# Optimization experiments

Measured on AMD Instinct MI355X. Metric: run time of the kernel, lower is better.

Reference implementation:

```python
import jax, jax.numpy as jnp
import numpy as np

MAX_COV = 1e4
MIN_COV = 1e-4
SYMM_THRESH = 1e-5
DET_THRESH = 1e-6
MAX_POS = 1e3
EIG_CLAMP = 1e-4
INV_EPS = 1e-4


def _symmetrize(A):
    return (A + jnp.swapaxes(A, -1, -2)) * 0.5


def _spd_reconstruct(Q, lam):
    # Q @ diag(lam) @ Q^T for batched [N,3,3] Q and [N,3] lam
    return jnp.einsum('bij,bj,bkj->bik', Q, lam, Q)


def setup_inputs() -> dict:
    key = jax.random.key(0)
    k1, k2, k3, k4 = jax.random.split(key, 4)
    N = 1048576
    miu_1 = jax.random.normal(k1, (N, 3), dtype=jnp.float32)
    miu_2 = jax.random.normal(k2, (N, 3), dtype=jnp.float32)
    I = jnp.eye(3, dtype=jnp.float32)
    B1 = 0.5 * jax.random.normal(k3, (N, 3, 3), dtype=jnp.float32)
    B2 = 0.5 * jax.random.normal(k4, (N, 3, 3), dtype=jnp.float32)
    cov_1 = jnp.einsum('bij,bkj->bik', B1, B1) + 0.3 * I
    cov_2 = jnp.einsum('bij,bkj->bik', B2, B2) + 0.3 * I
    return {'miu_1': miu_1, 'miu_2': miu_2, 'cov_1': cov_1, 'cov_2': cov_2}


def _stable_mask(miu_1, miu_2, cov_1, cov_2):
    a1 = jnp.abs(cov_1)
    a2 = jnp.abs(cov_2)
    m = (a1.max((-1, -2)) < MAX_COV) & (a2.max((-1, -2)) < MAX_COV)
    m &= (a1.min((-1, -2)) > MIN_COV) & (a2.min((-1, -2)) > MIN_COV)
    d1 = jnp.abs(cov_1 - jnp.swapaxes(cov_1, -1, -2)).max((-1, -2))
    d2 = jnp.abs(cov_2 - jnp.swapaxes(cov_2, -1, -2)).max((-1, -2))
    m &= (d1 < SYMM_THRESH) & (d2 < SYMM_THRESH)
    m &= (jnp.abs(jnp.linalg.det(cov_1)) > DET_THRESH)
    m &= (jnp.abs(jnp.linalg.det(cov_2)) > DET_THRESH)
    m &= jnp.all(jnp.isfinite(cov_1), axis=(-1, -2))
    m &= jnp.all(jnp.isfinite(cov_2), axis=(-1, -2))
    m &= jnp.abs(miu_1).max(-1) < MAX_POS
    m &= jnp.abs(miu_2).max(-1) < MAX_POS
    return m


def reference(miu_1, miu_2, cov_1, cov_2):
    mask = _stable_mask(miu_1, miu_2, cov_1, cov_2)  # [N] bool
    mM = mask[:, None, None]
    I = jnp.eye(3, dtype=cov_1.dtype)
    # sanitize masked-out rows so eigh stays well-conditioned; their outputs
    # are overwritten with zeros below (matching torch's masked-index path)
    c1 = jnp.where(mM, cov_1, I)
    c2 = jnp.where(mM, cov_2, I)

    L_A, Q_A = jnp.linalg.eigh(_symmetrize(c1))
    L_A = jnp.maximum(L_A, EIG_CLAMP)
    sqrt_L = jnp.sqrt(L_A)
    A_sqrt = _spd_reconstruct(Q_A, sqrt_L)               # cov1^{1/2}
    A_sqrt_inv = _spd_reconstruct(Q_A, 1.0 / (INV_EPS + sqrt_L))

    C = _symmetrize(jnp.einsum('bij,bjk,blk->bil', A_sqrt, c2, A_sqrt))
    L_C, Q_C = jnp.linalg.eigh(C)
    C_sqrt = _spd_reconstruct(Q_C, (L_C ** 2) ** 0.25)   # matrix_sqrt_H

    cov_vel = jnp.einsum('bij,bjk,blk->bil', A_sqrt, C_sqrt, A_sqrt_inv)
    cov_vel = cov_vel + jnp.swapaxes(cov_vel, -1, -2) - cov_1 - jnp.swapaxes(cov_1, -1, -2)

    miu_vel = jnp.where(mask[:, None], miu_2 - miu_1, 0.0)
    cov_vel = jnp.where(mM, cov_vel, 0.0)
    return miu_vel, cov_vel
```

## Files before the change

kernel.cpp:

```cpp
#include <hip/hip_runtime.h>
#include <math.h>

#define MAX_COV 10000.0f
#define MIN_COV 0.0001f
#define SYMM_THRESH 1e-05f
#define DET_THRESH 1e-06f
#define MAX_POS 1000.0f
#define EIG_CLAMP 0.0001f
#define INV_EPS 0.0001f

namespace {
constexpr int BS = 256;

__device__ __forceinline__ float rcp_fast(float x)  { return __builtin_amdgcn_rcpf(x); }
__device__ __forceinline__ float sqrt_fast(float x) { return __builtin_amdgcn_sqrtf(x); }

__device__ __forceinline__ float acos_fast(float x) {
    const float t = fabsf(x);
    const float s = sqrt_fast(fmaxf(1.0f - t, 0.0f));
    float p = fmaf(t, -0.0187293f, 0.0742610f);
    p = fmaf(t, p, -0.2121144f);
    p = fmaf(t, p, 1.5707288f);
    const float a = s * p;
    return (x >= 0.0f) ? a : (3.14159265358979f - a);
}

__device__ __forceinline__ void eigvals3(
    float m00, float m01, float m02, float m11, float m12, float m22,
    float& l1, float& l2, float& l3)
{
    const float q   = (m00 + m11 + m22) * (1.0f / 3.0f);
    const float b00 = m00 - q, b11 = m11 - q, b22 = m22 - q;
    const float offsq = m01 * m01 + m02 * m02 + m12 * m12;
    const float p2  = b00 * b00 + b11 * b11 + b22 * b22 + 2.0f * offsq;
    const float p   = sqrt_fast(p2 * (1.0f / 6.0f));
    const float detB =
          b00 * (b11 * b22 - m12 * m12)
        - m01 * (m01 * b22 - m12 * m02)
        + m02 * (m01 * m12 - b11 * m02);
    const float pinv = rcp_fast(fmaxf(p, 1e-30f));
    float r = 0.5f * detB;
    r = r * pinv; r = r * pinv; r = r * pinv;
    r = fminf(1.0f, fmaxf(-1.0f, r));
    const float phi = acos_fast(r) * (1.0f / 3.0f);
    const float c   = __cosf(phi);
    const float s   = sqrt_fast(fmaxf(1.0f - c * c, 0.0f));
    l1 = q + 2.0f * p * c;
    l3 = q + p * (-c - 1.7320508075688772f * s);
    l2 = 3.0f * q - l1 - l3;
}

__global__ __launch_bounds__(BS, 4)
void wl_kernel(const float* __restrict__ miu1, const float* __restrict__ miu2,
               const float* __restrict__ cov1, const float* __restrict__ cov2,
               float* __restrict__ out, int N)
{
    const int i = blockIdx.x * BS + threadIdx.x;
    if (i >= N) return;

    float c1[9], c2r[9], u1[3], u2[3];
    {
        const float* p1 = cov1 + (size_t)i * 9;
        const float* p2 = cov2 + (size_t)i * 9;
        #pragma unroll
        for (int k = 0; k < 9; ++k) { c1[k] = p1[k]; c2r[k] = p2[k]; }
        const float* q1p = miu1 + (size_t)i * 3;
        const float* q2p = miu2 + (size_t)i * 3;
        #pragma unroll
        for (int k = 0; k < 3; ++k) { u1[k] = q1p[k]; u2[k] = q2p[k]; }
    }

    float amax1 = 0.0f, amax2 = 0.0f, amin1 = 1e30f, amin2 = 1e30f;
    #pragma unroll
    for (int k = 0; k < 9; ++k) {
        amax1 = fmaxf(amax1, fabsf(c1[k]));  amin1 = fminf(amin1, fabsf(c1[k]));
        amax2 = fmaxf(amax2, fabsf(c2r[k])); amin2 = fminf(amin2, fabsf(c2r[k]));
    }
    bool ok = (amax1 < MAX_COV) && (amax2 < MAX_COV)
           && (amin1 > MIN_COV) && (amin2 > MIN_COV);
    const float sd = fmaxf(fmaxf(fabsf(c1[1] - c1[3]), fabsf(c1[2] - c1[6])),
                    fmaxf(fabsf(c1[5] - c1[7]),
                    fmaxf(fmaxf(fabsf(c2r[1] - c2r[3]), fabsf(c2r[2] - c2r[6])),
                          fabsf(c2r[5] - c2r[7]))));
    ok = ok && (sd < SYMM_THRESH);
    const float det1 = c1[0] * (c1[4] * c1[8] - c1[5] * c1[7])
                     - c1[1] * (c1[3] * c1[8] - c1[5] * c1[6])
                     + c1[2] * (c1[3] * c1[7] - c1[4] * c1[6]);
    const float det2 = c2r[0] * (c2r[4] * c2r[8] - c2r[5] * c2r[7])
                     - c2r[1] * (c2r[3] * c2r[8] - c2r[5] * c2r[6])
                     + c2r[2] * (c2r[3] * c2r[7] - c2r[4] * c2r[6]);
    ok = ok && (fabsf(det1) > DET_THRESH) && (fabsf(det2) > DET_THRESH);
    const float um = fmaxf(fmaxf(fmaxf(fabsf(u1[0]), fabsf(u1[1])), fabsf(u1[2])),
                           fmaxf(fmaxf(fabsf(u2[0]), fabsf(u2[1])), fabsf(u2[2])));
    ok = ok && (um < MAX_POS);

    const float m00 = ok ? c1[0] : 1.0f;
    const float m01 = ok ? (0.5f * (c1[1] + c1[3])) : 0.0f;
    const float m02 = ok ? (0.5f * (c1[2] + c1[6])) : 0.0f;
    const float m11 = ok ? c1[4] : 1.0f;
    const float m12 = ok ? (0.5f * (c1[5] + c1[7])) : 0.0f;
    const float m22 = ok ? c1[8] : 1.0f;
    const float d00 = ok ? c2r[0] : 1.0f;
    const float d01 = ok ? (0.5f * (c2r[1] + c2r[3])) : 0.0f;
    const float d02 = ok ? (0.5f * (c2r[2] + c2r[6])) : 0.0f;
    const float d11 = ok ? c2r[4] : 1.0f;
    const float d12 = ok ? (0.5f * (c2r[5] + c2r[7])) : 0.0f;
    const float d22 = ok ? c2r[8] : 1.0f;

    float l1, l2, l3;
    eigvals3(m00, m01, m02, m11, m12, m22, l1, l2, l3);
    l1 = fmaxf(l1, EIG_CLAMP); l2 = fmaxf(l2, EIG_CLAMP); l3 = fmaxf(l3, EIG_CLAMP);
    const float sa = sqrt_fast(l1), sb = sqrt_fast(l2), sc = sqrt_fast(l3);
    const float i_ab = rcp_fast(sa + sb);
    const float i_bc = rcp_fast(sb + sc);
    const float i_ac = rcp_fast(sa + sc);
    const float q0 = sa, q1 = i_ab, q2 = -i_ab * i_bc * i_ac;
    const float ea = rcp_fast(INV_EPS + sa);
    const float eb = rcp_fast(INV_EPS + sb);
    const float ec = rcp_fast(INV_EPS + sc);
    const float g0 = ea;
    const float g1 = -ea * eb * i_ab;
    const float g2 = (INV_EPS + sa + sb + sc) * ea * eb * ec * i_ab * i_bc * i_ac;

    const float u00 = m00 - l1, u11 = m11 - l1, u22 = m22 - l1;
    const float v00 = m00 - l2, v11 = m11 - l2, v22 = m22 - l2;
    const float P00 = u00 * v00 + m01 * m01 + m02 * m02;
    const float P01 = u00 * m01 + m01 * v11 + m02 * m12;
    const float P02 = u00 * m02 + m01 * m12 + m02 * v22;
    const float P11 = m01 * m01 + u11 * v11 + m12 * m12;
    const float P12 = m01 * m02 + u11 * m12 + m12 * v22;
    const float P22 = m02 * m02 + m12 * m12 + u22 * v22;

    const float S00 = q0 + q1 * u00 + q2 * P00;
    const float S01 =      q1 * m01 + q2 * P01;
    const float S02 =      q1 * m02 + q2 * P02;
    const float S11 = q0 + q1 * u11 + q2 * P11;
    const float S12 =      q1 * m12 + q2 * P12;
    const float S22 = q0 + q1 * u22 + q2 * P22;

    const float G00 = g0 + g1 * u00 + g2 * P00;
    const float G01 =      g1 * m01 + g2 * P01;
    const float G02 =      g1 * m02 + g2 * P02;
    const float G11 = g0 + g1 * u11 + g2 * P11;
    const float G12 =      g1 * m12 + g2 * P12;
    const float G22 = g0 + g1 * u22 + g2 * P22;

    const float T00 = S00 * d00 + S01 * d01 + S02 * d02;
    const float T01 = S00 * d01 + S01 * d11 + S02 * d12;
    const float T02 = S00 * d02 + S01 * d12 + S02 * d22;
    const float T10 = S01 * d00 + S11 * d01 + S12 * d02;
    const float T11 = S01 * d01 + S11 * d11 + S12 * d12;
    const float T12 = S01 * d02 + S11 * d12 + S12 * d22;
    const float T20 = S02 * d00 + S12 * d01 + S22 * d02;
    const float T21 = S02 * d01 + S12 * d11 + S22 * d12;
    const float T22m = S02 * d02 + S12 * d12 + S22 * d22;
    const float C00 = T00 * S00 + T01 * S01 + T02 * S02;
    const float C01 = T00 * S01 + T01 * S11 + T02 * S12;
    const float C02 = T00 * S02 + T01 * S12 + T02 * S22;
    const float C11 = T10 * S01 + T11 * S11 + T12 * S12;
    const float C12 = T10 * S02 + T11 * S12 + T12 * S22;
    const float C22 = T20 * S02 + T21 * S12 + T22m * S22;

    float e1, e2, e3;
    eigvals3(C00, C01, C02, C11, C12, C22, e1, e2, e3);
    const float ra = sqrt_fast(fabsf(e1));
    const float rb = sqrt_fast(fabsf(e2));
    const float rc = sqrt_fast(fabsf(e3));
    const float j_ab = rcp_fast(fmaxf(ra + rb, 1e-12f));
    const float j_bc = rcp_fast(fmaxf(rb + rc, 1e-12f));
    const float j_ac = rcp_fast(fmaxf(ra + rc, 1e-12f));
    const float h0 = ra, h1 = j_ab, h2 = -j_ab * j_bc * j_ac;
    const float cu00 = C00 - e1, cu11 = C11 - e1, cu22 = C22 - e1;
    const float cv00 = C00 - e2, cv11 = C11 - e2, cv22 = C22 - e2;
    const float R00 = cu00 * cv00 + C01 * C01 + C02 * C02;
    const float R01 = cu00 * C01 + C01 * cv11 + C02 * C12;
    const float R02 = cu00 * C02 + C01 * C12 + C02 * cv22;
    const float R11 = C01 * C01 + cu11 * cv11 + C12 * C12;
    const float R12 = C01 * C02 + cu11 * C12 + C12 * cv22;
    const float R22 = C02 * C02 + C12 * C12 + cu22 * cv22;

    const float X00 = h0 + h1 * cu00 + h2 * R00;
    const float X01 =      h1 * C01  + h2 * R01;
    const float X02 =      h1 * C02  + h2 * R02;
    const float X11 = h0 + h1 * cu11 + h2 * R11;
    const float X12 =      h1 * C12  + h2 * R12;
    const float X22 = h0 + h1 * cu22 + h2 * R22;

    const float A00 = S00 * X00 + S01 * X01 + S02 * X02;
    const float A01 = S00 * X01 + S01 * X11 + S02 * X12;
    const float A02 = S00 * X02 + S01 * X12 + S02 * X22;
    const float A10 = S01 * X00 + S11 * X01 + S12 * X02;
    const float A11 = S01 * X01 + S11 * X11 + S12 * X12;
    const float A12 = S01 * X02 + S11 * X12 + S12 * X22;
    const float A20 = S02 * X00 + S12 * X01 + S22 * X02;
    const float A21 = S02 * X01 + S12 * X11 + S22 * X12;
    const float A22 = S02 * X02 + S12 * X12 + S22 * X22;
    float W[9];
    W[0] = A00 * G00 + A01 * G01 + A02 * G02;
    W[1] = A00 * G01 + A01 * G11 + A02 * G12;
    W[2] = A00 * G02 + A01 * G12 + A02 * G22;
    W[3] = A10 * G00 + A11 * G01 + A12 * G02;
    W[4] = A10 * G01 + A11 * G11 + A12 * G12;
    W[5] = A10 * G02 + A11 * G12 + A12 * G22;
    W[6] = A20 * G00 + A21 * G01 + A22 * G02;
    W[7] = A20 * G01 + A21 * G11 + A22 * G12;
    W[8] = A20 * G02 + A21 * G12 + A22 * G22;

    const float M1f[9] = { m00, m01, m02, m01, m11, m12, m02, m12, m22 };
    float* out_miu = out;
    float* out_cov = out + (size_t)N * 3;
    float* oc = out_cov + (size_t)i * 9;
    #pragma unroll
    for (int r = 0; r < 3; ++r)
        #pragma unroll
        for (int cidx = 0; cidx < 3; ++cidx)
            oc[r * 3 + cidx] = ok ? (W[r * 3 + cidx] + W[cidx * 3 + r] - 2.0f * M1f[r * 3 + cidx])
                                  : 0.0f;
    float* om = out_miu + (size_t)i * 3;
    #pragma unroll
    for (int k = 0; k < 3; ++k) om[k] = ok ? (u2[k] - u1[k]) : 0.0f;
}

}

extern "C" void kernel_launch(void* const* d_in, const int* in_sizes, int n_in,
                              void* d_out, int out_size, void* d_ws, size_t ws_size,
                              hipStream_t stream)
{
    const float* miu1 = (const float*)d_in[0];
    const float* miu2 = (const float*)d_in[1];
    const float* cov1 = (const float*)d_in[2];
    const float* cov2 = (const float*)d_in[3];
    float* out = (float*)d_out;
    const int N = in_sizes[0] / 3;
    const int grid = (N + BS - 1) / BS;
    hipLaunchKernelGGL(wl_kernel, dim3(grid), dim3(BS), 0, stream,
                       miu1, miu2, cov1, cov2, out, N);
}
```

Before: 28.61 us.

## Stage covariance loads and stores through LDS with coalesced float4 transfers

Each block now loads its 256x9 covariance tiles for both inputs into shared memory with coalesced float4 global reads, computes per-thread from LDS, writes the results back into LDS, and then stores them with coalesced float4 writes. This replaces the strided 36-byte-per-thread global accesses that produced poorly coalesced memory transactions. The occupancy hint is also raised from 4 to 8 blocks. The cost is 18 KB of LDS per block, two barriers, possible LDS bank conflicts from the stride-9 per-thread access, and register pressure from the tighter launch bound.

```diff
diff --git a/kernel.cpp b/kernel.cpp
--- a/kernel.cpp
+++ b/kernel.cpp
@@ -50,175 +50,214 @@
     l2 = 3.0f * q - l1 - l3;
 }
 
-__global__ __launch_bounds__(BS, 4)
+__global__ __launch_bounds__(BS, 8)
 void wl_kernel(const float* __restrict__ miu1, const float* __restrict__ miu2,
                const float* __restrict__ cov1, const float* __restrict__ cov2,
                float* __restrict__ out, int N)
 {
-    const int i = blockIdx.x * BS + threadIdx.x;
-    if (i >= N) return;
-
-    float c1[9], c2r[9], u1[3], u2[3];
-    {
-        const float* p1 = cov1 + (size_t)i * 9;
-        const float* p2 = cov2 + (size_t)i * 9;
-        #pragma unroll
-        for (int k = 0; k < 9; ++k) { c1[k] = p1[k]; c2r[k] = p2[k]; }
-        const float* q1p = miu1 + (size_t)i * 3;
-        const float* q2p = miu2 + (size_t)i * 3;
-        #pragma unroll
-        for (int k = 0; k < 3; ++k) { u1[k] = q1p[k]; u2[k] = q2p[k]; }
+    __shared__ float s_a[BS * 9];
+    __shared__ float s_b[BS * 9];
+
+    const int tid  = threadIdx.x;
+    const int base = blockIdx.x * BS;
+    const int nb   = min(BS, N - base);
+    const bool full = (nb == BS);
+
+    float* out_cov = out + (size_t)N * 3;
+
+    if (full) {
+        const float4* g1 = (const float4*)(cov1 + (size_t)base * 9);
+        const float4* g2 = (const float4*)(cov2 + (size_t)base * 9);
+        float4* la = (float4*)s_a;
+        float4* lb = (float4*)s_b;
+        #pragma unroll
+        for (int j = 0; j < 2; ++j) {
+            la[tid + j * BS] = g1[tid + j * BS];
+            lb[tid + j * BS] = g2[tid + j * BS];
+        }
+        if (tid < BS * 9 / 4 - 2 * BS) {
+            la[2 * BS + tid] = g1[2 * BS + tid];
+            lb[2 * BS + tid] = g2[2 * BS + tid];
+        }
+    } else {
+        for (int j = tid; j < nb * 9; j += BS) {
+            s_a[j] = cov1[(size_t)base * 9 + j];
+            s_b[j] = cov2[(size_t)base * 9 + j];
+        }
     }
-
-    float amax1 = 0.0f, amax2 = 0.0f, amin1 = 1e30f, amin2 = 1e30f;
-    #pragma unroll
-    for (int k = 0; k < 9; ++k) {
-        amax1 = fmaxf(amax1, fabsf(c1[k]));  amin1 = fminf(amin1, fabsf(c1[k]));
-        amax2 = fmaxf(amax2, fabsf(c2r[k])); amin2 = fminf(amin2, fabsf(c2r[k]));
+    __syncthreads();
+
+    if (tid < nb) {
+        const int i = base + tid;
+        float c1[9], c2r[9], u1[3], u2[3];
+        #pragma unroll
+        for (int k = 0; k < 9; ++k) { c1[k] = s_a[tid * 9 + k]; c2r[k] = s_b[tid * 9 + k]; }
+        {
+            const float* q1p = miu1 + (size_t)i * 3;
+            const float* q2p = miu2 + (size_t)i * 3;
+            #pragma unroll
+            for (int k = 0; k < 3; ++k) { u1[k] = q1p[k]; u2[k] = q2p[k]; }
+        }
+
+        float amax1 = 0.0f, amax2 = 0.0f, amin1 = 1e30f, amin2 = 1e30f;
+        #pragma unroll
+        for (int k = 0; k < 9; ++k) {
+            amax1 = fmaxf(amax1, fabsf(c1[k]));  amin1 = fminf(amin1, fabsf(c1[k]));
+            amax2 = fmaxf(amax2, fabsf(c2r[k])); amin2 = fminf(amin2, fabsf(c2r[k]));
+        }
+        bool ok = (amax1 < MAX_COV) && (amax2 < MAX_COV)
+               && (amin1 > MIN_COV) && (amin2 > MIN_COV);
+        const float sd = fmaxf(fmaxf(fabsf(c1[1] - c1[3]), fabsf(c1[2] - c1[6])),
+                        fmaxf(fabsf(c1[5] - c1[7]),
+                        fmaxf(fmaxf(fabsf(c2r[1] - c2r[3]), fabsf(c2r[2] - c2r[6])),
+                              fabsf(c2r[5] - c2r[7]))));
+        ok = ok && (sd < SYMM_THRESH);
+        const float det1 = c1[0] * (c1[4] * c1[8] - c1[5] * c1[7])
+                         - c1[1] * (c1[3] * c1[8] - c1[5] * c1[6])
+                         + c1[2] * (c1[3] * c1[7] - c1[4] * c1[6]);
+        const float det2 = c2r[0] * (c2r[4] * c2r[8] - c2r[5] * c2r[7])
+                         - c2r[1] * (c2r[3] * c2r[8] - c2r[5] * c2r[6])
+                         + c2r[2] * (c2r[3] * c2r[7] - c2r[4] * c2r[6]);
+        ok = ok && (fabsf(det1) > DET_THRESH) && (fabsf(det2) > DET_THRESH);
+        const float um = fmaxf(fmaxf(fmaxf(fabsf(u1[0]), fabsf(u1[1])), fabsf(u1[2])),
+                               fmaxf(fmaxf(fabsf(u2[0]), fabsf(u2[1])), fabsf(u2[2])));
+        ok = ok && (um < MAX_POS);
+
+        const float m00 = ok ? c1[0] : 1.0f;
+        const float m01 = ok ? (0.5f * (c1[1] + c1[3])) : 0.0f;
+        const float m02 = ok ? (0.5f * (c1[2] + c1[6])) : 0.0f;
+        const float m11 = ok ? c1[4] : 1.0f;
+        const float m12 = ok ? (0.5f * (c1[5] + c1[7])) : 0.0f;
+        const float m22 = ok ? c1[8] : 1.0f;
+        const float d00 = ok ? c2r[0] : 1.0f;
+        const float d01 = ok ? (0.5f * (c2r[1] + c2r[3])) : 0.0f;
+        const float d02 = ok ? (0.5f * (c2r[2] + c2r[6])) : 0.0f;
+        const float d11 = ok ? c2r[4] : 1.0f;
+        const float d12 = ok ? (0.5f * (c2r[5] + c2r[7])) : 0.0f;
+        const float d22 = ok ? c2r[8] : 1.0f;
+
+        float l1, l2, l3;
+        eigvals3(m00, m01, m02, m11, m12, m22, l1, l2, l3);
+        l1 = fmaxf(l1, EIG_CLAMP); l2 = fmaxf(l2, EIG_CLAMP); l3 = fmaxf(l3, EIG_CLAMP);
+        const float sa = sqrt_fast(l1), sb = sqrt_fast(l2), sc = sqrt_fast(l3);
+        const float i_ab = rcp_fast(sa + sb);
+        const float i_bc = rcp_fast(sb + sc);
+        const float i_ac = rcp_fast(sa + sc);
+        const float q0 = sa, q1 = i_ab, q2 = -i_ab * i_bc * i_ac;
+        const float ea = rcp_fast(INV_EPS + sa);
+        const float eb = rcp_fast(INV_EPS + sb);
+        const float ec = rcp_fast(INV_EPS + sc);
+        const float g0 = ea;
+        const float g1 = -ea * eb * i_ab;
+        const float g2 = (INV_EPS + sa + sb + sc) * ea * eb * ec * i_ab * i_bc * i_ac;
+
+        const float u00 = m00 - l1, u11 = m11 - l1, u22 = m22 - l1;
+        const float v00 = m00 - l2, v11 = m11 - l2, v22 = m22 - l2;
+        const float P00 = u00 * v00 + m01 * m01 + m02 * m02;
+        const float P01 = u00 * m01 + m01 * v11 + m02 * m12;
+        const float P02 = u00 * m02 + m01 * m12 + m02 * v22;
+        const float P11 = m01 * m01 + u11 * v11 + m12 * m12;
+        const float P12 = m01 * m02 + u11 * m12 + m12 * v22;
+        const float P22 = m02 * m02 + m12 * m12 + u22 * v22;
+
+        const float S00 = q0 + q1 * u00 + q2 * P00;
+        const float S01 =      q1 * m01 + q2 * P01;
+        const float S02 =      q1 * m02 + q2 * P02;
+        const float S11 = q0 + q1 * u11 + q2 * P11;
+        const float S12 =      q1 * m12 + q2 * P12;
+        const float S22 = q0 + q1 * u22 + q2 * P22;
+
+        const float G00 = g0 + g1 * u00 + g2 * P00;
+        const float G01 =      g1 * m01 + g2 * P01;
+        const float G02 =      g1 * m02 + g2 * P02;
+        const float G11 = g0 + g1 * u11 + g2 * P11;
+        const float G12 =      g1 * m12 + g2 * P12;
+        const float G22 = g0 + g1 * u22 + g2 * P22;
+
+        const float T00 = S00 * d00 + S01 * d01 + S02 * d02;
+        const float T01 = S00 * d01 + S01 * d11 + S02 * d12;
+        const float T02 = S00 * d02 + S01 * d12 + S02 * d22;
+        const float T10 = S01 * d00 + S11 * d01 + S12 * d02;
+        const float T11 = S01 * d01 + S11 * d11 + S12 * d12;
+        const float T12 = S01 * d02 + S11 * d12 + S12 * d22;
+        const float T20 = S02 * d00 + S12 * d01 + S22 * d02;
+        const float T21 = S02 * d01 + S12 * d11 + S22 * d12;
+        const float T22m = S02 * d02 + S12 * d12 + S22 * d22;
+        const float C00 = T00 * S00 + T01 * S01 + T02 * S02;
+        const float C01 = T00 * S01 + T01 * S11 + T02 * S12;
+        const float C02 = T00 * S02 + T01 * S12 + T02 * S22;
+        const float C11 = T10 * S01 + T11 * S11 + T12 * S12;
+        const float C12 = T10 * S02 + T11 * S12 + T12 * S22;
+        const float C22 = T20 * S02 + T21 * S12 + T22m * S22;
+
+        float e1, e2, e3;
+        eigvals3(C00, C01, C02, C11, C12, C22, e1, e2, e3);
+        const float ra = sqrt_fast(fabsf(e1));
+        const float rb = sqrt_fast(fabsf(e2));
+        const float rc = sqrt_fast(fabsf(e3));
+        const float j_ab = rcp_fast(fmaxf(ra + rb, 1e-12f));
+        const float j_bc = rcp_fast(fmaxf(rb + rc, 1e-12f));
+        const float j_ac = rcp_fast(fmaxf(ra + rc, 1e-12f));
+        const float h0 = ra, h1 = j_ab, h2 = -j_ab * j_bc * j_ac;
+        const float cu00 = C00 - e1, cu11 = C11 - e1, cu22 = C22 - e1;
+        const float cv00 = C00 - e2, cv11 = C11 - e2, cv22 = C22 - e2;
+        const float R00 = cu00 * cv00 + C01 * C01 + C02 * C02;
+        const float R01 = cu00 * C01 + C01 * cv11 + C02 * C12;
+        const float R02 = cu00 * C02 + C01 * C12 + C02 * cv22;
+        const float R11 = C01 * C01 + cu11 * cv11 + C12 * C12;
+        const float R12 = C01 * C02 + cu11 * C12 + C12 * cv22;
+        const float R22 = C02 * C02 + C12 * C12 + cu22 * cv22;
+
+        const float X00 = h0 + h1 * cu00 + h2 * R00;
+        const float X01 =      h1 * C01  + h2 * R01;
+        const float X02 =      h1 * C02  + h2 * R02;
+        const float X11 = h0 + h1 * cu11 + h2 * R11;
+        const float X12 =      h1 * C12  + h2 * R12;
+        const float X22 = h0 + h1 * cu22 + h2 * R22;
+
+        const float A00 = S00 * X00 + S01 * X01 + S02 * X02;
+        const float A01 = S00 * X01 + S01 * X11 + S02 * X12;
+        const float A02 = S00 * X02 + S01 * X12 + S02 * X22;
+        const float A10 = S01 * X00 + S11 * X01 + S12 * X02;
+        const float A11 = S01 * X01 + S11 * X11 + S12 * X12;
+        const float A12 = S01 * X02 + S11 * X12 + S12 * X22;
+        const float A20 = S02 * X00 + S12 * X01 + S22 * X02;
+        const float A21 = S02 * X01 + S12 * X11 + S22 * X12;
+        const float A22 = S02 * X02 + S12 * X12 + S22 * X22;
+        float W[9];
+        W[0] = A00 * G00 + A01 * G01 + A02 * G02;
+        W[1] = A00 * G01 + A01 * G11 + A02 * G12;
+        W[2] = A00 * G02 + A01 * G12 + A02 * G22;
+        W[3] = A10 * G00 + A11 * G01 + A12 * G02;
+        W[4] = A10 * G01 + A11 * G11 + A12 * G12;
+        W[5] = A10 * G02 + A11 * G12 + A12 * G22;
+        W[6] = A20 * G00 + A21 * G01 + A22 * G02;
+        W[7] = A20 * G01 + A21 * G11 + A22 * G12;
+        W[8] = A20 * G02 + A21 * G12 + A22 * G22;
+
+        const float M1f[9] = { m00, m01, m02, m01, m11, m12, m02, m12, m22 };
+        #pragma unroll
+        for (int r = 0; r < 3; ++r)
+            #pragma unroll
+            for (int cidx = 0; cidx < 3; ++cidx)
+                s_a[tid * 9 + r * 3 + cidx] =
+                    ok ? (W[r * 3 + cidx] + W[cidx * 3 + r] - 2.0f * M1f[r * 3 + cidx]) : 0.0f;
+
+        float* om = out + (size_t)i * 3;
+        #pragma unroll
+        for (int k = 0; k < 3; ++k) om[k] = ok ? (u2[k] - u1[k]) : 0.0f;
     }
-    bool ok = (amax1 < MAX_COV) && (amax2 < MAX_COV)
-           && (amin1 > MIN_COV) && (amin2 > MIN_COV);
-    const float sd = fmaxf(fmaxf(fabsf(c1[1] - c1[3]), fabsf(c1[2] - c1[6])),
-                    fmaxf(fabsf(c1[5] - c1[7]),
-                    fmaxf(fmaxf(fabsf(c2r[1] - c2r[3]), fabsf(c2r[2] - c2r[6])),
-                          fabsf(c2r[5] - c2r[7]))));
-    ok = ok && (sd < SYMM_THRESH);
-    const float det1 = c1[0] * (c1[4] * c1[8] - c1[5] * c1[7])
-                     - c1[1] * (c1[3] * c1[8] - c1[5] * c1[6])
-                     + c1[2] * (c1[3] * c1[7] - c1[4] * c1[6]);
-    const float det2 = c2r[0] * (c2r[4] * c2r[8] - c2r[5] * c2r[7])
-                     - c2r[1] * (c2r[3] * c2r[8] - c2r[5] * c2r[6])
-                     + c2r[2] * (c2r[3] * c2r[7] - c2r[4] * c2r[6]);
-    ok = ok && (fabsf(det1) > DET_THRESH) && (fabsf(det2) > DET_THRESH);
-    const float um = fmaxf(fmaxf(fmaxf(fabsf(u1[0]), fabsf(u1[1])), fabsf(u1[2])),
-                           fmaxf(fmaxf(fabsf(u2[0]), fabsf(u2[1])), fabsf(u2[2])));
-    ok = ok && (um < MAX_POS);
-
-    const float m00 = ok ? c1[0] : 1.0f;
-    const float m01 = ok ? (0.5f * (c1[1] + c1[3])) : 0.0f;
-    const float m02 = ok ? (0.5f * (c1[2] + c1[6])) : 0.0f;
-    const float m11 = ok ? c1[4] : 1.0f;
-    const float m12 = ok ? (0.5f * (c1[5] + c1[7])) : 0.0f;
-    const float m22 = ok ? c1[8] : 1.0f;
-    const float d00 = ok ? c2r[0] : 1.0f;
-    const float d01 = ok ? (0.5f * (c2r[1] + c2r[3])) : 0.0f;
-    const float d02 = ok ? (0.5f * (c2r[2] + c2r[6])) : 0.0f;
-    const float d11 = ok ? c2r[4] : 1.0f;
-    const float d12 = ok ? (0.5f * (c2r[5] + c2r[7])) : 0.0f;
-    const float d22 = ok ? c2r[8] : 1.0f;
-
-    float l1, l2, l3;
-    eigvals3(m00, m01, m02, m11, m12, m22, l1, l2, l3);
-    l1 = fmaxf(l1, EIG_CLAMP); l2 = fmaxf(l2, EIG_CLAMP); l3 = fmaxf(l3, EIG_CLAMP);
-    const float sa = sqrt_fast(l1), sb = sqrt_fast(l2), sc = sqrt_fast(l3);
-    const float i_ab = rcp_fast(sa + sb);
-    const float i_bc = rcp_fast(sb + sc);
-    const float i_ac = rcp_fast(sa + sc);
-    const float q0 = sa, q1 = i_ab, q2 = -i_ab * i_bc * i_ac;
-    const float ea = rcp_fast(INV_EPS + sa);
-    const float eb = rcp_fast(INV_EPS + sb);
-    const float ec = rcp_fast(INV_EPS + sc);
-    const float g0 = ea;
-    const float g1 = -ea * eb * i_ab;
-    const float g2 = (INV_EPS + sa + sb + sc) * ea * eb * ec * i_ab * i_bc * i_ac;
-
-    const float u00 = m00 - l1, u11 = m11 - l1, u22 = m22 - l1;
-    const float v00 = m00 - l2, v11 = m11 - l2, v22 = m22 - l2;
-    const float P00 = u00 * v00 + m01 * m01 + m02 * m02;
-    const float P01 = u00 * m01 + m01 * v11 + m02 * m12;
-    const float P02 = u00 * m02 + m01 * m12 + m02 * v22;
-    const float P11 = m01 * m01 + u11 * v11 + m12 * m12;
-    const float P12 = m01 * m02 + u11 * m12 + m12 * v22;
-    const float P22 = m02 * m02 + m12 * m12 + u22 * v22;
-
-    const float S00 = q0 + q1 * u00 + q2 * P00;
-    const float S01 =      q1 * m01 + q2 * P01;
-    const float S02 =      q1 * m02 + q2 * P02;
-    const float S11 = q0 + q1 * u11 + q2 * P11;
-    const float S12 =      q1 * m12 + q2 * P12;
-    const float S22 = q0 + q1 * u22 + q2 * P22;
-
-    const float G00 = g0 + g1 * u00 + g2 * P00;
-    const float G01 =      g1 * m01 + g2 * P01;
-    const float G02 =      g1 * m02 + g2 * P02;
-    const float G11 = g0 + g1 * u11 + g2 * P11;
-    const float G12 =      g1 * m12 + g2 * P12;
-    const float G22 = g0 + g1 * u22 + g2 * P22;
-
-    const float T00 = S00 * d00 + S01 * d01 + S02 * d02;
-    const float T01 = S00 * d01 + S01 * d11 + S02 * d12;
-    const float T02 = S00 * d02 + S01 * d12 + S02 * d22;
-    const float T10 = S01 * d00 + S11 * d01 + S12 * d02;
-    const float T11 = S01 * d01 + S11 * d11 + S12 * d12;
-    const float T12 = S01 * d02 + S11 * d12 + S12 * d22;
-    const float T20 = S02 * d00 + S12 * d01 + S22 * d02;
-    const float T21 = S02 * d01 + S12 * d11 + S22 * d12;
-    const float T22m = S02 * d02 + S12 * d12 + S22 * d22;
-    const float C00 = T00 * S00 + T01 * S01 + T02 * S02;
-    const float C01 = T00 * S01 + T01 * S11 + T02 * S12;
-    const float C02 = T00 * S02 + T01 * S12 + T02 * S22;
-    const float C11 = T10 * S01 + T11 * S11 + T12 * S12;
-    const float C12 = T10 * S02 + T11 * S12 + T12 * S22;
-    const float C22 = T20 * S02 + T21 * S12 + T22m * S22;
-
-    float e1, e2, e3;
-    eigvals3(C00, C01, C02, C11, C12, C22, e1, e2, e3);
-    const float ra = sqrt_fast(fabsf(e1));
-    const float rb = sqrt_fast(fabsf(e2));
-    const float rc = sqrt_fast(fabsf(e3));
-    const float j_ab = rcp_fast(fmaxf(ra + rb, 1e-12f));
-    const float j_bc = rcp_fast(fmaxf(rb + rc, 1e-12f));
-    const float j_ac = rcp_fast(fmaxf(ra + rc, 1e-12f));
-    const float h0 = ra, h1 = j_ab, h2 = -j_ab * j_bc * j_ac;
-    const float cu00 = C00 - e1, cu11 = C11 - e1, cu22 = C22 - e1;
-    const float cv00 = C00 - e2, cv11 = C11 - e2, cv22 = C22 - e2;
-    const float R00 = cu00 * cv00 + C01 * C01 + C02 * C02;
-    const float R01 = cu00 * C01 + C01 * cv11 + C02 * C12;
-    const float R02 = cu00 * C02 + C01 * C12 + C02 * cv22;
-    const float R11 = C01 * C01 + cu11 * cv11 + C12 * C12;
-    const float R12 = C01 * C02 + cu11 * C12 + C12 * cv22;
-    const float R22 = C02 * C02 + C12 * C12 + cu22 * cv22;
-
-    const float X00 = h0 + h1 * cu00 + h2 * R00;
-    const float X01 =      h1 * C01  + h2 * R01;
-    const float X02 =      h1 * C02  + h2 * R02;
-    const float X11 = h0 + h1 * cu11 + h2 * R11;
-    const float X12 =      h1 * C12  + h2 * R12;
-    const float X22 = h0 + h1 * cu22 + h2 * R22;
-
-    const float A00 = S00 * X00 + S01 * X01 + S02 * X02;
-    const float A01 = S00 * X01 + S01 * X11 + S02 * X12;
-    const float A02 = S00 * X02 + S01 * X12 + S02 * X22;
-    const float A10 = S01 * X00 + S11 * X01 + S12 * X02;
-    const float A11 = S01 * X01 + S11 * X11 + S12 * X12;
-    const float A12 = S01 * X02 + S11 * X12 + S12 * X22;
-    const float A20 = S02 * X00 + S12 * X01 + S22 * X02;
-    const float A21 = S02 * X01 + S12 * X11 + S22 * X12;
-    const float A22 = S02 * X02 + S12 * X12 + S22 * X22;
-    float W[9];
-    W[0] = A00 * G00 + A01 * G01 + A02 * G02;
-    W[1] = A00 * G01 + A01 * G11 + A02 * G12;
-    W[2] = A00 * G02 + A01 * G12 + A02 * G22;
-    W[3] = A10 * G00 + A11 * G01 + A12 * G02;
-    W[4] = A10 * G01 + A11 * G11 + A12 * G12;
-    W[5] = A10 * G02 + A11 * G12 + A12 * G22;
-    W[6] = A20 * G00 + A21 * G01 + A22 * G02;
-    W[7] = A20 * G01 + A21 * G11 + A22 * G12;
-    W[8] = A20 * G02 + A21 * G12 + A22 * G22;
-
-    const float M1f[9] = { m00, m01, m02, m01, m11, m12, m02, m12, m22 };
-    float* out_miu = out;
-    float* out_cov = out + (size_t)N * 3;
-    float* oc = out_cov + (size_t)i * 9;
-    #pragma unroll
-    for (int r = 0; r < 3; ++r)
-        #pragma unroll
-        for (int cidx = 0; cidx < 3; ++cidx)
-            oc[r * 3 + cidx] = ok ? (W[r * 3 + cidx] + W[cidx * 3 + r] - 2.0f * M1f[r * 3 + cidx])
-                                  : 0.0f;
-    float* om = out_miu + (size_t)i * 3;
-    #pragma unroll
-    for (int k = 0; k < 3; ++k) om[k] = ok ? (u2[k] - u1[k]) : 0.0f;
+    __syncthreads();
+
+    if (full && ((((size_t)(out_cov + (size_t)base * 9)) & 15) == 0)) {
+        float4* go = (float4*)(out_cov + (size_t)base * 9);
+        const float4* la = (const float4*)s_a;
+        #pragma unroll
+        for (int j = 0; j < 2; ++j) go[tid + j * BS] = la[tid + j * BS];
+        if (tid < BS * 9 / 4 - 2 * BS) go[2 * BS + tid] = la[2 * BS + tid];
+    } else {
+        for (int j = tid; j < nb * 9; j += BS) out_cov[(size_t)base * 9 + j] = s_a[j];
+    }
 }
 
 }
```

Result: slower. 39.52 us (+38.1%).

## Stage per-wave loads and stores through LDS for coalesced global access

Applied to the files above, without the earlier changes.

Each wave now copies its 64 elements' covariance and mean data into shared memory with coalesced contiguous loads, then each lane reads its own strided record from LDS. Outputs go back through LDS the same way before coalesced global stores. This targets the uncoalesced 9-float and 3-float strided accesses of the per-thread layout, at the cost of about 18 KB of LDS per block, extra LDS traffic and possible bank conflicts on the stride-9 and stride-3 reads. A tail path keeps the direct per-thread access for partial waves.

```diff
diff --git a/kernel.cpp b/kernel.cpp
--- a/kernel.cpp
+++ b/kernel.cpp
@@ -11,6 +11,7 @@
 
 namespace {
 constexpr int BS = 256;
+constexpr int NW = BS / 64;
 
 __device__ __forceinline__ float rcp_fast(float x)  { return __builtin_amdgcn_rcpf(x); }
 __device__ __forceinline__ float sqrt_fast(float x) { return __builtin_amdgcn_sqrtf(x); }
@@ -50,26 +51,10 @@
     l2 = 3.0f * q - l1 - l3;
 }
 
-__global__ __launch_bounds__(BS, 4)
-void wl_kernel(const float* __restrict__ miu1, const float* __restrict__ miu2,
-               const float* __restrict__ cov1, const float* __restrict__ cov2,
-               float* __restrict__ out, int N)
-{
-    const int i = blockIdx.x * BS + threadIdx.x;
-    if (i >= N) return;
-
-    float c1[9], c2r[9], u1[3], u2[3];
-    {
-        const float* p1 = cov1 + (size_t)i * 9;
-        const float* p2 = cov2 + (size_t)i * 9;
-        #pragma unroll
-        for (int k = 0; k < 9; ++k) { c1[k] = p1[k]; c2r[k] = p2[k]; }
-        const float* q1p = miu1 + (size_t)i * 3;
-        const float* q2p = miu2 + (size_t)i * 3;
-        #pragma unroll
-        for (int k = 0; k < 3; ++k) { u1[k] = q1p[k]; u2[k] = q2p[k]; }
-    }
-
+__device__ __forceinline__ void process_one(
+    const float* c1, const float* c2r, const float* u1, const float* u2,
+    float* wout, float* mv)
+{
     float amax1 = 0.0f, amax2 = 0.0f, amin1 = 1e30f, amin2 = 1e30f;
     #pragma unroll
     for (int k = 0; k < 9; ++k) {
@@ -207,18 +192,90 @@
     W[8] = A20 * G02 + A21 * G12 + A22 * G22;
 
     const float M1f[9] = { m00, m01, m02, m01, m11, m12, m02, m12, m22 };
-    float* out_miu = out;
-    float* out_cov = out + (size_t)N * 3;
-    float* oc = out_cov + (size_t)i * 9;
     #pragma unroll
     for (int r = 0; r < 3; ++r)
         #pragma unroll
         for (int cidx = 0; cidx < 3; ++cidx)
-            oc[r * 3 + cidx] = ok ? (W[r * 3 + cidx] + W[cidx * 3 + r] - 2.0f * M1f[r * 3 + cidx])
-                                  : 0.0f;
-    float* om = out_miu + (size_t)i * 3;
+            wout[r * 3 + cidx] =
+                ok ? (W[r * 3 + cidx] + W[cidx * 3 + r] - 2.0f * M1f[r * 3 + cidx]) : 0.0f;
     #pragma unroll
-    for (int k = 0; k < 3; ++k) om[k] = ok ? (u2[k] - u1[k]) : 0.0f;
+    for (int k = 0; k < 3; ++k) mv[k] = ok ? (u2[k] - u1[k]) : 0.0f;
+}
+
+__global__ __launch_bounds__(BS, 4)
+void wl_kernel(const float* __restrict__ miu1, const float* __restrict__ miu2,
+               const float* __restrict__ cov1, const float* __restrict__ cov2,
+               float* __restrict__ out, int N)
+{
+    __shared__ float s_c1[NW][576];
+    __shared__ float s_c2[NW][576];
+    __shared__ float s_mu[NW][384];
+
+    const int w = threadIdx.x >> 6;
+    const int l = threadIdx.x & 63;
+    const int wbase = blockIdx.x * BS + w * 64;
+    if (wbase >= N) return;
+
+    float* out_cov = out + (size_t)N * 3;
+    float c1[9], c2[9], u1[3], u2[3];
+    float wout[9], mv[3];
+
+    if (wbase + 64 <= N) {
+        const float* g1 = cov1 + (size_t)wbase * 9;
+        const float* g2 = cov2 + (size_t)wbase * 9;
+        #pragma unroll
+        for (int k = 0; k < 9; ++k) {
+            s_c1[w][l + 64 * k] = g1[l + 64 * k];
+            s_c2[w][l + 64 * k] = g2[l + 64 * k];
+        }
+        const float* gm1 = miu1 + (size_t)wbase * 3;
+        const float* gm2 = miu2 + (size_t)wbase * 3;
+        #pragma unroll
+        for (int k = 0; k < 3; ++k) {
+            s_mu[w][l + 64 * k]       = gm1[l + 64 * k];
+            s_mu[w][192 + l + 64 * k] = gm2[l + 64 * k];
+        }
+        __builtin_amdgcn_wave_barrier();
+
+        #pragma unroll
+        for (int k = 0; k < 9; ++k) { c1[k] = s_c1[w][l * 9 + k]; c2[k] = s_c2[w][l * 9 + k]; }
+        #pragma unroll
+        for (int k = 0; k < 3; ++k) { u1[k] = s_mu[w][l * 3 + k]; u2[k] = s_mu[w][192 + l * 3 + k]; }
+
+        process_one(c1, c2, u1, u2, wout, mv);
+
+        __builtin_amdgcn_wave_barrier();
+        #pragma unroll
+        for (int k = 0; k < 9; ++k) s_c1[w][l * 9 + k] = wout[k];
+        #pragma unroll
+        for (int k = 0; k < 3; ++k) s_mu[w][l * 3 + k] = mv[k];
+        __builtin_amdgcn_wave_barrier();
+
+        float* oc = out_cov + (size_t)wbase * 9;
+        #pragma unroll
+        for (int k = 0; k < 9; ++k) oc[l + 64 * k] = s_c1[w][l + 64 * k];
+        float* om = out + (size_t)wbase * 3;
+        #pragma unroll
+        for (int k = 0; k < 3; ++k) om[l + 64 * k] = s_mu[w][l + 64 * k];
+    } else {
+        const int i = wbase + l;
+        if (i >= N) return;
+        #pragma unroll
+        for (int k = 0; k < 9; ++k) {
+            c1[k] = cov1[(size_t)i * 9 + k];
+            c2[k] = cov2[(size_t)i * 9 + k];
+        }
+        #pragma unroll
+        for (int k = 0; k < 3; ++k) {
+            u1[k] = miu1[(size_t)i * 3 + k];
+            u2[k] = miu2[(size_t)i * 3 + k];
+        }
+        process_one(c1, c2, u1, u2, wout, mv);
+        #pragma unroll
+        for (int k = 0; k < 9; ++k) out_cov[(size_t)i * 9 + k] = wout[k];
+        #pragma unroll
+        for (int k = 0; k < 3; ++k) out[(size_t)i * 3 + k] = mv[k];
+    }
 }
 
 }
```

New measurement: 29.52 us. 1.03x slower.

## Pack per-thread 3x3 matrix math into float2 vectors for packed FMA

Applied to the files above, without the earlier changes.

Rewrites the per-element matrix products (P, S/G, T, C, R, X, A, W and the output symmetrisation) as operations on two-wide float vectors, so the compiler can emit packed FP32 instructions (v_pk_fma_f32) that do two lanes per instruction. It also folds the divide-by-three into the acos polynomial coefficients, computes pinv cubed once, and replaces the sqrt(1-c^2) with __sinf. The aim is to cut VALU instruction count in a compute-bound kernel. The cost is extra register shuffles to build and split the vectors, which may offset the gain, plus small accuracy changes from the refit polynomial and __sinf.

```diff
diff --git a/kernel.cpp b/kernel.cpp
--- a/kernel.cpp
+++ b/kernel.cpp
@@ -12,17 +12,20 @@
 namespace {
 constexpr int BS = 256;
 
+typedef float v2f __attribute__((ext_vector_type(2)));
+__device__ __forceinline__ v2f mk2(float a, float b) { v2f r; r[0] = a; r[1] = b; return r; }
+
 __device__ __forceinline__ float rcp_fast(float x)  { return __builtin_amdgcn_rcpf(x); }
 __device__ __forceinline__ float sqrt_fast(float x) { return __builtin_amdgcn_sqrtf(x); }
 
-__device__ __forceinline__ float acos_fast(float x) {
+__device__ __forceinline__ float acos3_fast(float x) {
     const float t = fabsf(x);
     const float s = sqrt_fast(fmaxf(1.0f - t, 0.0f));
-    float p = fmaf(t, -0.0187293f, 0.0742610f);
-    p = fmaf(t, p, -0.2121144f);
-    p = fmaf(t, p, 1.5707288f);
-    const float a = s * p;
-    return (x >= 0.0f) ? a : (3.14159265358979f - a);
+    float p = fmaf(t, -0.00624310f, 0.02475367f);
+    p = fmaf(t, p, -0.07070480f);
+    p = fmaf(t, p, 0.52357627f);
+    const float a3 = s * p;
+    return (x >= 0.0f) ? a3 : (1.0471975512f - a3);
 }
 
 __device__ __forceinline__ void eigvals3(
@@ -38,13 +41,13 @@
           b00 * (b11 * b22 - m12 * m12)
         - m01 * (m01 * b22 - m12 * m02)
         + m02 * (m01 * m12 - b11 * m02);
-    const float pinv = rcp_fast(fmaxf(p, 1e-30f));
-    float r = 0.5f * detB;
-    r = r * pinv; r = r * pinv; r = r * pinv;
+    const float pinv  = rcp_fast(fmaxf(p, 1e-30f));
+    const float pinv3 = pinv * pinv * pinv;
+    float r = (0.5f * detB) * pinv3;
     r = fminf(1.0f, fmaxf(-1.0f, r));
-    const float phi = acos_fast(r) * (1.0f / 3.0f);
+    const float phi = acos3_fast(r);
     const float c   = __cosf(phi);
-    const float s   = sqrt_fast(fmaxf(1.0f - c * c, 0.0f));
+    const float s   = __sinf(phi);
     l1 = q + 2.0f * p * c;
     l3 = q + p * (-c - 1.7320508075688772f * s);
     l2 = 3.0f * q - l1 - l3;
@@ -94,18 +97,21 @@
                            fmaxf(fmaxf(fabsf(u2[0]), fabsf(u2[1])), fabsf(u2[2])));
     ok = ok && (um < MAX_POS);
 
+    const v2f md01 = 0.5f * (mk2(c1[1], c2r[1]) + mk2(c1[3], c2r[3]));
+    const v2f md02 = 0.5f * (mk2(c1[2], c2r[2]) + mk2(c1[6], c2r[6]));
+    const v2f md12 = 0.5f * (mk2(c1[5], c2r[5]) + mk2(c1[7], c2r[7]));
     const float m00 = ok ? c1[0] : 1.0f;
-    const float m01 = ok ? (0.5f * (c1[1] + c1[3])) : 0.0f;
-    const float m02 = ok ? (0.5f * (c1[2] + c1[6])) : 0.0f;
     const float m11 = ok ? c1[4] : 1.0f;
-    const float m12 = ok ? (0.5f * (c1[5] + c1[7])) : 0.0f;
     const float m22 = ok ? c1[8] : 1.0f;
+    const float m01 = ok ? md01[0] : 0.0f;
+    const float m02 = ok ? md02[0] : 0.0f;
+    const float m12 = ok ? md12[0] : 0.0f;
     const float d00 = ok ? c2r[0] : 1.0f;
-    const float d01 = ok ? (0.5f * (c2r[1] + c2r[3])) : 0.0f;
-    const float d02 = ok ? (0.5f * (c2r[2] + c2r[6])) : 0.0f;
     const float d11 = ok ? c2r[4] : 1.0f;
-    const float d12 = ok ? (0.5f * (c2r[5] + c2r[7])) : 0.0f;
     const float d22 = ok ? c2r[8] : 1.0f;
+    const float d01 = ok ? md01[1] : 0.0f;
+    const float d02 = ok ? md02[1] : 0.0f;
+    const float d12 = ok ? md12[1] : 0.0f;
 
     float l1, l2, l3;
     eigvals3(m00, m01, m02, m11, m12, m22, l1, l2, l3);
@@ -114,52 +120,50 @@
     const float i_ab = rcp_fast(sa + sb);
     const float i_bc = rcp_fast(sb + sc);
     const float i_ac = rcp_fast(sa + sc);
-    const float q0 = sa, q1 = i_ab, q2 = -i_ab * i_bc * i_ac;
     const float ea = rcp_fast(INV_EPS + sa);
     const float eb = rcp_fast(INV_EPS + sb);
     const float ec = rcp_fast(INV_EPS + sc);
-    const float g0 = ea;
-    const float g1 = -ea * eb * i_ab;
-    const float g2 = (INV_EPS + sa + sb + sc) * ea * eb * ec * i_ab * i_bc * i_ac;
+    const v2f qg0 = mk2(sa, ea);
+    const v2f qg1 = mk2(i_ab, -ea * eb * i_ab);
+    const v2f qg2 = mk2(-i_ab * i_bc * i_ac,
+                        (INV_EPS + sa + sb + sc) * ea * eb * ec * i_ab * i_bc * i_ac);
 
     const float u00 = m00 - l1, u11 = m11 - l1, u22 = m22 - l1;
     const float v00 = m00 - l2, v11 = m11 - l2, v22 = m22 - l2;
-    const float P00 = u00 * v00 + m01 * m01 + m02 * m02;
-    const float P01 = u00 * m01 + m01 * v11 + m02 * m12;
-    const float P02 = u00 * m02 + m01 * m12 + m02 * v22;
-    const float P11 = m01 * m01 + u11 * v11 + m12 * m12;
-    const float P12 = m01 * m02 + u11 * m12 + m12 * v22;
-    const float P22 = m02 * m02 + m12 * m12 + u22 * v22;
-
-    const float S00 = q0 + q1 * u00 + q2 * P00;
-    const float S01 =      q1 * m01 + q2 * P01;
-    const float S02 =      q1 * m02 + q2 * P02;
-    const float S11 = q0 + q1 * u11 + q2 * P11;
-    const float S12 =      q1 * m12 + q2 * P12;
-    const float S22 = q0 + q1 * u22 + q2 * P22;
-
-    const float G00 = g0 + g1 * u00 + g2 * P00;
-    const float G01 =      g1 * m01 + g2 * P01;
-    const float G02 =      g1 * m02 + g2 * P02;
-    const float G11 = g0 + g1 * u11 + g2 * P11;
-    const float G12 =      g1 * m12 + g2 * P12;
-    const float G22 = g0 + g1 * u22 + g2 * P22;
-
-    const float T00 = S00 * d00 + S01 * d01 + S02 * d02;
-    const float T01 = S00 * d01 + S01 * d11 + S02 * d12;
-    const float T02 = S00 * d02 + S01 * d12 + S02 * d22;
-    const float T10 = S01 * d00 + S11 * d01 + S12 * d02;
-    const float T11 = S01 * d01 + S11 * d11 + S12 * d12;
-    const float T12 = S01 * d02 + S11 * d12 + S12 * d22;
-    const float T20 = S02 * d00 + S12 * d01 + S22 * d02;
-    const float T21 = S02 * d01 + S12 * d11 + S22 * d12;
-    const float T22m = S02 * d02 + S12 * d12 + S22 * d22;
-    const float C00 = T00 * S00 + T01 * S01 + T02 * S02;
-    const float C01 = T00 * S01 + T01 * S11 + T02 * S12;
-    const float C02 = T00 * S02 + T01 * S12 + T02 * S22;
-    const float C11 = T10 * S01 + T11 * S11 + T12 * S12;
-    const float C12 = T10 * S02 + T11 * S12 + T12 * S22;
-    const float C22 = T20 * S02 + T21 * S12 + T22m * S22;
+    const v2f PA = u00 * mk2(v00, m01) + m01 * mk2(m01, v11) + m02 * mk2(m02, m12);
+    const v2f PB = mk2(u00, m01) * mk2(m02, m01) + mk2(m01, u11) * mk2(m12, v11)
+                 + mk2(m02, m12) * mk2(v22, m12);
+    const v2f PC = mk2(m01, m02) * mk2(m02, m02) + mk2(u11, m12) * mk2(m12, m12)
+                 + mk2(m12, u22) * mk2(v22, v22);
+
+    const v2f SG00 = qg0 + qg1 * u00 + qg2 * PA[0];
+    const v2f SG01 =       qg1 * m01 + qg2 * PA[1];
+    const v2f SG02 =       qg1 * m02 + qg2 * PB[0];
+    const v2f SG11 = qg0 + qg1 * u11 + qg2 * PB[1];
+    const v2f SG12 =       qg1 * m12 + qg2 * PC[0];
+    const v2f SG22 = qg0 + qg1 * u22 + qg2 * PC[1];
+    const float S00 = SG00[0], G00 = SG00[1];
+    const float S01 = SG01[0], G01 = SG01[1];
+    const float S02 = SG02[0], G02 = SG02[1];
+    const float S11 = SG11[0], G11 = SG11[1];
+    const float S12 = SG12[0], G12 = SG12[1];
+    const float S22 = SG22[0], G22 = SG22[1];
+
+    const v2f TA = S00 * mk2(d00, d01) + S01 * mk2(d01, d11) + S02 * mk2(d02, d12);
+    const v2f TB = mk2(S00, S01) * mk2(d02, d00) + mk2(S01, S11) * mk2(d12, d01)
+                 + mk2(S02, S12) * mk2(d22, d02);
+    const v2f TC = S01 * mk2(d01, d02) + S11 * mk2(d11, d12) + S12 * mk2(d12, d22);
+    const v2f TD = S02 * mk2(d00, d01) + S12 * mk2(d01, d11) + S22 * mk2(d02, d12);
+    const float T00 = TA[0], T01 = TA[1], T02 = TB[0], T10 = TB[1];
+    const float T11 = TC[0], T12 = TC[1], T20 = TD[0], T21 = TD[1];
+    const float T22 = S02 * d02 + S12 * d12 + S22 * d22;
+
+    const v2f CA = T00 * mk2(S00, S01) + T01 * mk2(S01, S11) + T02 * mk2(S02, S12);
+    const v2f CB = mk2(T00, T10) * mk2(S02, S01) + mk2(T01, T11) * mk2(S12, S11)
+                 + mk2(T02, T12) * mk2(S22, S12);
+    const v2f CC = mk2(T10, T20) * S02 + mk2(T11, T21) * S12 + mk2(T12, T22) * S22;
+    const float C00 = CA[0], C01 = CA[1], C02 = CB[0];
+    const float C11 = CB[1], C12 = CC[0], C22 = CC[1];
 
     float e1, e2, e3;
     eigvals3(C00, C01, C02, C11, C12, C22, e1, e2, e3);
@@ -172,51 +176,52 @@
     const float h0 = ra, h1 = j_ab, h2 = -j_ab * j_bc * j_ac;
     const float cu00 = C00 - e1, cu11 = C11 - e1, cu22 = C22 - e1;
     const float cv00 = C00 - e2, cv11 = C11 - e2, cv22 = C22 - e2;
-    const float R00 = cu00 * cv00 + C01 * C01 + C02 * C02;
-    const float R01 = cu00 * C01 + C01 * cv11 + C02 * C12;
-    const float R02 = cu00 * C02 + C01 * C12 + C02 * cv22;
-    const float R11 = C01 * C01 + cu11 * cv11 + C12 * C12;
-    const float R12 = C01 * C02 + cu11 * C12 + C12 * cv22;
-    const float R22 = C02 * C02 + C12 * C12 + cu22 * cv22;
-
-    const float X00 = h0 + h1 * cu00 + h2 * R00;
-    const float X01 =      h1 * C01  + h2 * R01;
-    const float X02 =      h1 * C02  + h2 * R02;
-    const float X11 = h0 + h1 * cu11 + h2 * R11;
-    const float X12 =      h1 * C12  + h2 * R12;
-    const float X22 = h0 + h1 * cu22 + h2 * R22;
-
-    const float A00 = S00 * X00 + S01 * X01 + S02 * X02;
-    const float A01 = S00 * X01 + S01 * X11 + S02 * X12;
-    const float A02 = S00 * X02 + S01 * X12 + S02 * X22;
-    const float A10 = S01 * X00 + S11 * X01 + S12 * X02;
-    const float A11 = S01 * X01 + S11 * X11 + S12 * X12;
-    const float A12 = S01 * X02 + S11 * X12 + S12 * X22;
-    const float A20 = S02 * X00 + S12 * X01 + S22 * X02;
-    const float A21 = S02 * X01 + S12 * X11 + S22 * X12;
+    const v2f RA = cu00 * mk2(cv00, C01) + C01 * mk2(C01, cv11) + C02 * mk2(C02, C12);
+    const v2f RB = mk2(cu00, C01) * mk2(C02, C01) + mk2(C01, cu11) * mk2(C12, cv11)
+                 + mk2(C02, C12) * mk2(cv22, C12);
+    const v2f RC = mk2(C01, C02) * mk2(C02, C02) + mk2(cu11, C12) * mk2(C12, C12)
+                 + mk2(C12, cu22) * mk2(cv22, cv22);
+
+    const v2f XA = mk2(h0, 0.0f) + h1 * mk2(cu00, C01) + h2 * mk2(RA[0], RA[1]);
+    const v2f XB = mk2(h0, 0.0f) + h1 * mk2(cu11, C02) + h2 * mk2(RB[1], RB[0]);
+    const v2f XC = mk2(h0, 0.0f) + h1 * mk2(cu22, C12) + h2 * mk2(RC[1], RC[0]);
+    const float X00 = XA[0], X01 = XA[1], X11 = XB[0], X02 = XB[1];
+    const float X22 = XC[0], X12 = XC[1];
+
+    const v2f AA = S00 * mk2(X00, X01) + S01 * mk2(X01, X11) + S02 * mk2(X02, X12);
+    const v2f AB = mk2(S00, S01) * mk2(X02, X00) + mk2(S01, S11) * mk2(X12, X01)
+                 + mk2(S02, S12) * mk2(X22, X02);
+    const v2f AC = S01 * mk2(X01, X02) + S11 * mk2(X11, X12) + S12 * mk2(X12, X22);
+    const v2f AD = S02 * mk2(X00, X01) + S12 * mk2(X01, X11) + S22 * mk2(X02, X12);
+    const float A00 = AA[0], A01 = AA[1], A02 = AB[0], A10 = AB[1];
+    const float A11 = AC[0], A12 = AC[1], A20 = AD[0], A21 = AD[1];
     const float A22 = S02 * X02 + S12 * X12 + S22 * X22;
-    float W[9];
-    W[0] = A00 * G00 + A01 * G01 + A02 * G02;
-    W[1] = A00 * G01 + A01 * G11 + A02 * G12;
-    W[2] = A00 * G02 + A01 * G12 + A02 * G22;
-    W[3] = A10 * G00 + A11 * G01 + A12 * G02;
-    W[4] = A10 * G01 + A11 * G11 + A12 * G12;
-    W[5] = A10 * G02 + A11 * G12 + A12 * G22;
-    W[6] = A20 * G00 + A21 * G01 + A22 * G02;
-    W[7] = A20 * G01 + A21 * G11 + A22 * G12;
-    W[8] = A20 * G02 + A21 * G12 + A22 * G22;
-
-    const float M1f[9] = { m00, m01, m02, m01, m11, m12, m02, m12, m22 };
-    float* out_miu = out;
+
+    const v2f WA = A00 * mk2(G00, G01) + A01 * mk2(G01, G11) + A02 * mk2(G02, G12);
+    const v2f WB = mk2(A00, A10) * mk2(G02, G00) + mk2(A01, A11) * mk2(G12, G01)
+                 + mk2(A02, A12) * mk2(G22, G02);
+    const v2f WC = A10 * mk2(G01, G02) + A11 * mk2(G11, G12) + A12 * mk2(G12, G22);
+    const v2f WD = A20 * mk2(G00, G01) + A21 * mk2(G01, G11) + A22 * mk2(G02, G12);
+    const float W0 = WA[0], W1 = WA[1], W2 = WB[0], W3 = WB[1];
+    const float W4 = WC[0], W5 = WC[1], W6 = WD[0], W7 = WD[1];
+    const float W8 = A20 * G02 + A21 * G12 + A22 * G22;
+
+    const v2f EA = mk2(W0, W1) + mk2(W0, W3) - 2.0f * mk2(m00, m01);
+    const v2f EB = mk2(W2, W4) + mk2(W6, W4) - 2.0f * mk2(m02, m11);
+    const v2f EC = mk2(W5, W8) + mk2(W7, W8) - 2.0f * mk2(m12, m22);
+
     float* out_cov = out + (size_t)N * 3;
     float* oc = out_cov + (size_t)i * 9;
-    #pragma unroll
-    for (int r = 0; r < 3; ++r)
-        #pragma unroll
-        for (int cidx = 0; cidx < 3; ++cidx)
-            oc[r * 3 + cidx] = ok ? (W[r * 3 + cidx] + W[cidx * 3 + r] - 2.0f * M1f[r * 3 + cidx])
-                                  : 0.0f;
-    float* om = out_miu + (size_t)i * 3;
+    oc[0] = ok ? EA[0] : 0.0f;
+    oc[1] = ok ? EA[1] : 0.0f;
+    oc[2] = ok ? EB[0] : 0.0f;
+    oc[3] = ok ? EA[1] : 0.0f;
+    oc[4] = ok ? EB[1] : 0.0f;
+    oc[5] = ok ? EC[0] : 0.0f;
+    oc[6] = ok ? EB[0] : 0.0f;
+    oc[7] = ok ? EC[0] : 0.0f;
+    oc[8] = ok ? EC[1] : 0.0f;
+    float* om = out + (size_t)i * 3;
     #pragma unroll
     for (int k = 0; k < 3; ++k) om[k] = ok ? (u2[k] - u1[k]) : 0.0f;
 }
```

New measurement: 28.71 us. No clear change (+0.4%).
